# Kernel tuning notes

Hardware: AMD Instinct MI355X
Metric: run time of the kernel (lower is better)

## Reference

```python
import jax, jax.numpy as jnp
import numpy as np

N_HEADS = 4
NEG_SLOPE = 0.2  # DGL GATConv default leaky_relu slope


def setup_inputs() -> dict:
    key = jax.random.key(0)
    ks = jax.random.split(key, 12)
    N, E = 50000, 800000
    in_dim, time_dim, out_dim = 128, 128, 128
    d_head = out_dim // N_HEADS
    in_total = in_dim + time_dim
    h = jax.random.normal(ks[0], (N, in_dim), jnp.float32)
    time_tensor = jax.random.uniform(ks[1], (E,), jnp.float32)
    src = jax.random.randint(ks[2], (E,), 0, N, jnp.int32)
    dst = jax.random.randint(ks[3], (E,), 0, N, jnp.int32)
    # TimeEncoding: Linear(1, time_dim) with xavier weight, zero bias
    w_t = jax.random.normal(ks[4], (time_dim, 1), jnp.float32) * (6.0 / (1 + time_dim)) ** 0.5
    b_t = jnp.zeros((time_dim,), jnp.float32)
    # GATConv params
    W_fc = jax.random.normal(ks[5], (N_HEADS * d_head, in_total), jnp.float32) * (2.0 / in_total) ** 0.5
    attn_l = jax.random.normal(ks[6], (N_HEADS, d_head), jnp.float32) * 0.1
    attn_r = jax.random.normal(ks[7], (N_HEADS, d_head), jnp.float32) * 0.1
    W_res = jax.random.normal(ks[8], (N_HEADS * d_head, in_total), jnp.float32) * (2.0 / in_total) ** 0.5
    bias = jnp.zeros((N_HEADS * d_head,), jnp.float32)
    return {"h": h, "time_tensor": time_tensor, "src": src, "dst": dst,
            "num_nodes": N, "w_t": w_t, "b_t": b_t, "W_fc": W_fc,
            "attn_l": attn_l, "attn_r": attn_r, "W_res": W_res, "bias": bias}


def reference(h, time_tensor, src, dst, num_nodes, w_t, b_t, W_fc, attn_l, attn_r, W_res, bias):
    N = num_nodes
    E = src.shape[0]
    # Time encoding: cos(W t + b), per edge -> [E, time_dim]
    time_emb = jnp.cos(time_tensor[:, None] * w_t[:, 0][None, :] + b_t[None, :])
    # Mailbox mean of concat([src h, time_emb]) per dst node.
    # mean(concat) == concat(mean, mean), so sum the two halves separately.
    ones = jnp.ones((E,), h.dtype)
    deg = jax.ops.segment_sum(ones, dst, num_segments=N)  # [N]
    sum_h = jax.ops.segment_sum(h[src], dst, num_segments=N)       # [N, in_dim]
    sum_t = jax.ops.segment_sum(time_emb, dst, num_segments=N)     # [N, time_dim]
    inv_deg = 1.0 / jnp.maximum(deg, 1.0)
    h_time = jnp.concatenate([sum_h, sum_t], axis=1) * inv_deg[:, None]  # [N, in+time]
    # GATConv (eval mode, no dropout)
    d_head = W_fc.shape[0] // N_HEADS
    feat = (h_time @ W_fc.T).reshape(N, N_HEADS, d_head)  # [N,H,D]
    el = jnp.sum(feat * attn_l[None], axis=-1)  # [N,H]
    er = jnp.sum(feat * attn_r[None], axis=-1)  # [N,H]
    e = el[src] + er[dst]                        # [E,H]
    e = jnp.where(e > 0, e, NEG_SLOPE * e)
    # edge softmax over incoming edges of each dst node
    m = jax.ops.segment_max(e, dst, num_segments=N)  # [N,H]
    m = jnp.where(jnp.isfinite(m), m, 0.0)
    ex = jnp.exp(e - m[dst])
    denom = jax.ops.segment_sum(ex, dst, num_segments=N)
    a = ex / jnp.maximum(denom[dst], 1e-9)           # [E,H]
    rst = jax.ops.segment_sum(a[:, :, None] * feat[src], dst, num_segments=N)  # [N,H,D]
    res = (h_time @ W_res.T).reshape(N, N_HEADS, d_head)
    out = rst + res + bias.reshape(1, N_HEADS, d_head)
    out = jax.nn.elu(out)
    return out.reshape(N, -1)  # [N, out_dim]
```

## Files before the change

### kernel.cpp

```cpp
#include <hip/hip_runtime.h>
#include <math.h>

#define NH 4
#define NEG_SLOPE 0.2f
#define BKT_SHIFT 8
#define EPB 4096
#define CBLK 8192
#define INV2PI 0.15915494309189535f
#define LOG2E  1.4426950408889634f

typedef __attribute__((ext_vector_type(8))) short bf16x8;
typedef __attribute__((ext_vector_type(4))) float f32x4;

__device__ __forceinline__ float blo(unsigned u) { return __uint_as_float(u << 16); }
__device__ __forceinline__ float bhi(unsigned u) { return __uint_as_float(u & 0xFFFF0000u); }
__device__ __forceinline__ unsigned short rne(float f) {
    unsigned u = __float_as_uint(f);
    u += 0x7FFFu + ((u >> 16) & 1u);
    return (unsigned short)(u >> 16);
}
__device__ __forceinline__ unsigned pack2(float a, float b) {
    return (unsigned)rne(a) | ((unsigned)rne(b) << 16);
}

__global__ __launch_bounds__(256) void k_prep(
    const float* __restrict__ h, unsigned* __restrict__ hbu, int n_pairs,
    const float* __restrict__ Wfc, const float* __restrict__ Wres,
    unsigned* __restrict__ wcat,
    const float* __restrict__ w_t, const float* __restrict__ b_t,
    float2* __restrict__ w_s, float2* __restrict__ b_s) {
    int t = blockIdx.x * blockDim.x + threadIdx.x;
    if (t < n_pairs) {
        float2 v = ((const float2*)h)[t];
        hbu[t] = pack2(v.x, v.y);
    }
    if (t < 32768) {
        int col = t >> 7, kk = t & 127;
        const float* srcp = (col < 128) ? (Wfc + (size_t)col * 256)
                                        : (Wres + (size_t)(col - 128) * 256);
        float2 v = ((const float2*)srcp)[kk];
        wcat[t] = pack2(v.x, v.y);
    }
    if (t < 64) {
        float2 wv = ((const float2*)w_t)[t];
        float2 bv = ((const float2*)b_t)[t];
        w_s[t] = make_float2(wv.x * INV2PI, wv.y * INV2PI);
        b_s[t] = make_float2(bv.x * INV2PI, bv.y * INV2PI);
    }
}

__global__ __launch_bounds__(256) void k_bktcount(
    const int* __restrict__ dst, int* __restrict__ bkt_cnt, int E, int NB) {
    __shared__ int cnt[256];
    int tid = threadIdx.x;
    cnt[tid] = 0;
    __syncthreads();
    int q0 = (blockIdx.x * CBLK) >> 2;
#pragma unroll
    for (int k = 0; k < CBLK / 1024; k++) {
        int qi = q0 + k * 256 + tid;
        int base = qi * 4;
        if (base + 3 < E) {
            int4 d = ((const int4*)dst)[qi];
            atomicAdd(&cnt[d.x >> BKT_SHIFT], 1);
            atomicAdd(&cnt[d.y >> BKT_SHIFT], 1);
            atomicAdd(&cnt[d.z >> BKT_SHIFT], 1);
            atomicAdd(&cnt[d.w >> BKT_SHIFT], 1);
        } else {
            for (int e = base; e < E; e++) atomicAdd(&cnt[dst[e] >> BKT_SHIFT], 1);
        }
    }
    __syncthreads();
    if (tid < NB) {
        int c = cnt[tid];
        if (c) atomicAdd(bkt_cnt + tid, c);
    }
}

__global__ __launch_bounds__(256) void k_bktscan(
    const int* __restrict__ bkt_cnt, int* __restrict__ bkt_start,
    int* __restrict__ bkt_cursor, int* __restrict__ row_start,
    int NB, int E, int N) {
    __shared__ int wsum[4];
    int tid = threadIdx.x, lane = tid & 63, wid = tid >> 6;
    int v = (tid < NB) ? bkt_cnt[tid] : 0;
    int x = v;
#pragma unroll
    for (int off = 1; off < 64; off <<= 1) {
        int y = __shfl_up(x, off, 64);
        if (lane >= off) x += y;
    }
    if (lane == 63) wsum[wid] = x;
    __syncthreads();
    if (tid == 0) {
        int s = 0;
#pragma unroll
        for (int k = 0; k < 4; k++) { int tk = wsum[k]; wsum[k] = s; s += tk; }
    }
    __syncthreads();
    int excl = wsum[wid] + x - v;
    if (tid < NB) { bkt_start[tid] = excl; bkt_cursor[tid] = excl; }
    if (tid == 0) { bkt_start[NB] = E; row_start[N] = E; }
}

__global__ __launch_bounds__(256) void k_binscatter(
    const int* __restrict__ src, const int* __restrict__ dst,
    const float* __restrict__ tt, int* __restrict__ bkt_cursor,
    uint2* __restrict__ staged, int E, int NB) {
    __shared__ int cnt[1024];
    __shared__ int basep[1024];
    int e0 = blockIdx.x * EPB;
    int tid = threadIdx.x;
    for (int b = tid; b < NB; b += 256) cnt[b] = 0;
    __syncthreads();
#pragma unroll
    for (int k = 0; k < EPB / 256; k++) {
        int e = e0 + k * 256 + tid;
        if (e < E) atomicAdd(&cnt[dst[e] >> BKT_SHIFT], 1);
    }
    __syncthreads();
    for (int b = tid; b < NB; b += 256) {
        int c = cnt[b];
        basep[b] = (c > 0) ? atomicAdd(bkt_cursor + b, c) : 0;
        cnt[b] = 0;
    }
    __syncthreads();
#pragma unroll
    for (int k = 0; k < EPB / 256; k++) {
        int e = e0 + k * 256 + tid;
        if (e < E) {
            int d = dst[e];
            int b = d >> BKT_SHIFT;
            int r = atomicAdd(&cnt[b], 1);
            unsigned tq = min((unsigned)(tt[e] * 32768.0f), 32767u);
            staged[basep[b] + r] =
                make_uint2(((unsigned)src[e] << 15) | tq, (unsigned)(d & 255));
        }
    }
}

__global__ __launch_bounds__(256) void k_binsort(
    const uint2* __restrict__ staged, const int* __restrict__ bkt_start,
    int* __restrict__ row_start, unsigned* __restrict__ est, int N) {
    __shared__ int cnt[256];
    __shared__ int cur[256];
    __shared__ int wsum[4];
    int b = blockIdx.x;
    int n0 = b << BKT_SHIFT;
    int tid = threadIdx.x;
    cnt[tid] = 0;
    __syncthreads();
    int s0 = bkt_start[b], s1 = bkt_start[b + 1];
    for (int p = s0 + tid; p < s1; p += 256)
        atomicAdd(&cnt[staged[p].y], 1);
    __syncthreads();
    int lane = tid & 63, wid = tid >> 6;
    int v = cnt[tid];
    int x = v;
#pragma unroll
    for (int off = 1; off < 64; off <<= 1) {
        int y = __shfl_up(x, off, 64);
        if (lane >= off) x += y;
    }
    if (lane == 63) wsum[wid] = x;
    __syncthreads();
    if (tid == 0) {
        int s = 0;
#pragma unroll
        for (int k = 0; k < 4; k++) { int tk = wsum[k]; wsum[k] = s; s += tk; }
    }
    __syncthreads();
    int excl = s0 + wsum[wid] + x - v;
    cur[tid] = excl;
    if (n0 + tid < N) row_start[n0 + tid] = excl;
    __syncthreads();
    for (int p = s0 + tid; p < s1; p += 256) {
        uint2 vv = staged[p];
        int pos = atomicAdd(&cur[vv.y], 1);
        est[pos] = vv.x;
    }
}

__device__ __forceinline__ void agg_edge(unsigned u, float wgt, const uint4* __restrict__ h4,
                                         int i, float4 wa, float4 wb, float4 ba, float4 bb,
                                         float* aH, float* aT) {
    int s = (int)(u >> 15);
    float t = (float)((u & 0x7FFFu)) * (1.0f / 32768.0f) + (0.5f / 32768.0f);
    uint4 hv = h4[(size_t)s * 16 + i];
    aH[0] += wgt * blo(hv.x); aH[1] += wgt * bhi(hv.x);
    aH[2] += wgt * blo(hv.y); aH[3] += wgt * bhi(hv.y);
    aH[4] += wgt * blo(hv.z); aH[5] += wgt * bhi(hv.z);
    aH[6] += wgt * blo(hv.w); aH[7] += wgt * bhi(hv.w);
    aT[0] += wgt * __builtin_amdgcn_cosf(fmaf(t, wa.x, ba.x));
    aT[1] += wgt * __builtin_amdgcn_cosf(fmaf(t, wa.y, ba.y));
    aT[2] += wgt * __builtin_amdgcn_cosf(fmaf(t, wa.z, ba.z));
    aT[3] += wgt * __builtin_amdgcn_cosf(fmaf(t, wa.w, ba.w));
    aT[4] += wgt * __builtin_amdgcn_cosf(fmaf(t, wb.x, bb.x));
    aT[5] += wgt * __builtin_amdgcn_cosf(fmaf(t, wb.y, bb.y));
    aT[6] += wgt * __builtin_amdgcn_cosf(fmaf(t, wb.z, bb.z));
    aT[7] += wgt * __builtin_amdgcn_cosf(fmaf(t, wb.w, bb.w));
}

__device__ __forceinline__ void attn_edge(unsigned u, bool valid, const uint4* __restrict__ f4,
                                          int i, int hd, const float* __restrict__ el,
                                          float erh, float* acc, float& den) {
    int s = (int)(u >> 15);
    float elh = el[(size_t)s * 4 + hd];
    uint4 fv = f4[(size_t)s * 16 + i];
    float w = elh + erh; w = w > 0.f ? w : NEG_SLOPE * w;
    float ex = valid ? __builtin_amdgcn_exp2f(w) : 0.f;
    acc[0] = fmaf(ex, blo(fv.x), acc[0]); acc[1] = fmaf(ex, bhi(fv.x), acc[1]);
    acc[2] = fmaf(ex, blo(fv.y), acc[2]); acc[3] = fmaf(ex, bhi(fv.y), acc[3]);
    acc[4] = fmaf(ex, blo(fv.z), acc[4]); acc[5] = fmaf(ex, bhi(fv.z), acc[5]);
    acc[6] = fmaf(ex, blo(fv.w), acc[6]); acc[7] = fmaf(ex, bhi(fv.w), acc[7]);
    den += ex;
}

__global__ __launch_bounds__(256) void k_agg(
    const unsigned* __restrict__ hbu, const unsigned* __restrict__ est,
    const int* __restrict__ row_start,
    const float2* __restrict__ w_s, const float2* __restrict__ b_s,
    unsigned* __restrict__ htu, int N) {
    int n = blockIdx.x * 4 + (threadIdx.x >> 6);
    if (n >= N) return;
    int lane = threadIdx.x & 63;
    int g = lane >> 4, i = lane & 15;
    int rs = row_start[n], re = row_start[n + 1];
    const uint4* h4 = (const uint4*)hbu;
    float4 wa = ((const float4*)w_s)[2 * i], wb = ((const float4*)w_s)[2 * i + 1];
    float4 ba = ((const float4*)b_s)[2 * i], bb = ((const float4*)b_s)[2 * i + 1];
    float aH[8] = {}, aT[8] = {};
    for (int e = rs + g; e < re; e += 16) {
        int e1 = e + 4, e2 = e + 8, e3 = e + 12;
        bool v1 = e1 < re, v2 = e2 < re, v3 = e3 < re;
        unsigned u0 = est[e];
        unsigned u1 = est[v1 ? e1 : e];
        unsigned u2 = est[v2 ? e2 : e];
        unsigned u3 = est[v3 ? e3 : e];
        agg_edge(u0, 1.0f, h4, i, wa, wb, ba, bb, aH, aT);
        agg_edge(u1, v1 ? 1.0f : 0.0f, h4, i, wa, wb, ba, bb, aH, aT);
        agg_edge(u2, v2 ? 1.0f : 0.0f, h4, i, wa, wb, ba, bb, aH, aT);
        agg_edge(u3, v3 ? 1.0f : 0.0f, h4, i, wa, wb, ba, bb, aH, aT);
    }
#pragma unroll
    for (int off = 16; off <= 32; off <<= 1) {
#pragma unroll
        for (int k = 0; k < 8; k++) {
            aH[k] += __shfl_xor(aH[k], off, 64);
            aT[k] += __shfl_xor(aT[k], off, 64);
        }
    }
    if (g == 0) {
        int deg = re - rs;
        float idg = (deg > 0) ? 1.0f / (float)deg : 1.0f;
        uint4* ht4 = (uint4*)htu;
        uint4 oh, ot;
        oh.x = pack2(aH[0] * idg, aH[1] * idg);
        oh.y = pack2(aH[2] * idg, aH[3] * idg);
        oh.z = pack2(aH[4] * idg, aH[5] * idg);
        oh.w = pack2(aH[6] * idg, aH[7] * idg);
        ot.x = pack2(aT[0] * idg, aT[1] * idg);
        ot.y = pack2(aT[2] * idg, aT[3] * idg);
        ot.z = pack2(aT[4] * idg, aT[5] * idg);
        ot.w = pack2(aT[6] * idg, aT[7] * idg);
        ht4[(size_t)n * 32 + i]      = oh;
        ht4[(size_t)n * 32 + 16 + i] = ot;
    }
}

__global__ __launch_bounds__(256) void k_gemm(
    const unsigned short* __restrict__ ht, const unsigned short* __restrict__ wcat,
    unsigned short* __restrict__ feat, float* __restrict__ res_out, int N) {
    __shared__ __align__(16) unsigned short As[64 * 264];
    int tid = threadIdx.x;
    int row0 = blockIdx.x * 64;
    const uint4* src4 = (const uint4*)ht;
    for (int idx = tid; idx < 64 * 32; idx += 256) {
        int rl = idx >> 5, c16 = idx & 31;
        int gr = row0 + rl; if (gr >= N) gr = N - 1;
        uint4 v = src4[(size_t)gr * 32 + c16];
        *(uint4*)(As + rl * 264 + c16 * 8) = v;
    }
    __syncthreads();
    int wave = tid >> 6, lane = tid & 63;
    int r = lane & 15, q = lane >> 4;
    int colbase = wave * 64;
    const bf16x8* bbase = (const bf16x8*)wcat + (size_t)(colbase + r) * 32;
    const unsigned short* abase = As + r * 264 + q * 8;
    f32x4 acc[4][4] = {};
#pragma unroll
    for (int ks = 0; ks < 8; ks++) {
        bf16x8 a[4], b[4];
#pragma unroll
        for (int rt = 0; rt < 4; rt++)
            a[rt] = *(const bf16x8*)(abase + rt * (16 * 264) + ks * 32);
#pragma unroll
        for (int ct = 0; ct < 4; ct++)
            b[ct] = bbase[(size_t)ct * (16 * 32) + ks * 4 + q];
#pragma unroll
        for (int rt = 0; rt < 4; rt++)
#pragma unroll
            for (int ct = 0; ct < 4; ct++)
                acc[rt][ct] = __builtin_amdgcn_mfma_f32_16x16x32_bf16(a[rt], b[ct], acc[rt][ct], 0, 0, 0);
    }
#pragma unroll
    for (int rt = 0; rt < 4; rt++) {
        int rb = row0 + rt * 16 + q * 4;
#pragma unroll
        for (int ct = 0; ct < 4; ct++) {
            int col = colbase + ct * 16 + r;
#pragma unroll
            for (int reg = 0; reg < 4; reg++) {
                int row = rb + reg;
                if (row >= N) continue;
                float v = acc[rt][ct][reg];
                if (col < 128) feat[(size_t)row * 128 + col] = rne(v);
                else           res_out[(size_t)row * 128 + (col - 128)] = v;
            }
        }
    }
}

__global__ void k_el_er(const unsigned* __restrict__ featu,
                        const float* __restrict__ attn_l, const float* __restrict__ attn_r,
                        float* __restrict__ el, float* __restrict__ er, int NH4) {
    int t = blockIdx.x * blockDim.x + threadIdx.x;
    if (t >= NH4) return;
    int n = t >> 2, hd = t & 3;
    const unsigned* f = featu + (size_t)n * 64 + hd * 16;
    const float2* al = (const float2*)(attn_l + hd * 32);
    const float2* ar = (const float2*)(attn_r + hd * 32);
    float sl = 0.f, sr = 0.f;
#pragma unroll
    for (int i = 0; i < 16; i++) {
        unsigned u = f[i];
        float f0 = blo(u), f1 = bhi(u);
        float2 a = al[i], b = ar[i];
        sl = fmaf(f0, a.x, fmaf(f1, a.y, sl));
        sr = fmaf(f0, b.x, fmaf(f1, b.y, sr));
    }
    el[t] = sl * LOG2E;
    er[t] = sr * LOG2E;
}

__global__ __launch_bounds__(256) void k_attn(
    const unsigned* __restrict__ est, const int* __restrict__ row_start,
    const float* __restrict__ el, const float* __restrict__ er,
    const unsigned* __restrict__ featu, const float* __restrict__ bias,
    float* __restrict__ out, int N) {
    int n = blockIdx.x * 4 + (threadIdx.x >> 6);
    if (n >= N) return;
    int lane = threadIdx.x & 63;
    int g = lane >> 4, i = lane & 15;
    int hd = i >> 2;
    int rs = row_start[n], re = row_start[n + 1];
    float erh = er[(size_t)n * 4 + hd];
    const uint4* f4 = (const uint4*)featu;
    float acc[8] = {};
    float den = 0.f;
    for (int e = rs + g; e < re; e += 16) {
        int e1 = e + 4, e2 = e + 8, e3 = e + 12;
        bool v1 = e1 < re, v2 = e2 < re, v3 = e3 < re;
        unsigned u0 = est[e];
        unsigned u1 = est[v1 ? e1 : e];
        unsigned u2 = est[v2 ? e2 : e];
        unsigned u3 = est[v3 ? e3 : e];
        attn_edge(u0, true, f4, i, hd, el, erh, acc, den);
        attn_edge(u1, v1, f4, i, hd, el, erh, acc, den);
        attn_edge(u2, v2, f4, i, hd, el, erh, acc, den);
        attn_edge(u3, v3, f4, i, hd, el, erh, acc, den);
    }
#pragma unroll
    for (int off = 16; off <= 32; off <<= 1) {
#pragma unroll
        for (int k = 0; k < 8; k++) acc[k] += __shfl_xor(acc[k], off, 64);
        den += __shfl_xor(den, off, 64);
    }
    if (g == 0) {
        float id = 1.0f / fmaxf(den, 1e-9f);
        float* op = out + (size_t)n * 128 + i * 8;
        const float* bp = bias + i * 8;
        float4 o0 = ((const float4*)op)[0], o1 = ((const float4*)op)[1];
        float4 b0 = ((const float4*)bp)[0], b1 = ((const float4*)bp)[1];
        float4 r0, r1;
        r0.x = fmaf(acc[0], id, o0.x + b0.x);
        r0.y = fmaf(acc[1], id, o0.y + b0.y);
        r0.z = fmaf(acc[2], id, o0.z + b0.z);
        r0.w = fmaf(acc[3], id, o0.w + b0.w);
        r1.x = fmaf(acc[4], id, o1.x + b1.x);
        r1.y = fmaf(acc[5], id, o1.y + b1.y);
        r1.z = fmaf(acc[6], id, o1.z + b1.z);
        r1.w = fmaf(acc[7], id, o1.w + b1.w);
        r0.x = r0.x > 0.f ? r0.x : (__expf(r0.x) - 1.0f);
        r0.y = r0.y > 0.f ? r0.y : (__expf(r0.y) - 1.0f);
        r0.z = r0.z > 0.f ? r0.z : (__expf(r0.z) - 1.0f);
        r0.w = r0.w > 0.f ? r0.w : (__expf(r0.w) - 1.0f);
        r1.x = r1.x > 0.f ? r1.x : (__expf(r1.x) - 1.0f);
        r1.y = r1.y > 0.f ? r1.y : (__expf(r1.y) - 1.0f);
        r1.z = r1.z > 0.f ? r1.z : (__expf(r1.z) - 1.0f);
        r1.w = r1.w > 0.f ? r1.w : (__expf(r1.w) - 1.0f);
        ((float4*)op)[0] = r0;
        ((float4*)op)[1] = r1;
    }
}

extern "C" void kernel_launch(void* const* d_in, const int* in_sizes, int n_in,
                              void* d_out, int out_size, void* d_ws, size_t ws_size,
                              hipStream_t stream) {
    const float* h     = (const float*)d_in[0];
    const float* tt    = (const float*)d_in[1];
    const int*   src   = (const int*)d_in[2];
    const int*   dst   = (const int*)d_in[3];
    const float* w_t   = (const float*)d_in[5];
    const float* b_t   = (const float*)d_in[6];
    const float* W_fc  = (const float*)d_in[7];
    const float* al    = (const float*)d_in[8];
    const float* ar    = (const float*)d_in[9];
    const float* W_res = (const float*)d_in[10];
    const float* bias  = (const float*)d_in[11];

    int N = in_sizes[0] / 128;
    int E = in_sizes[1];
    int NB = (N + 255) >> BKT_SHIFT;

    char* ws = (char*)d_ws;
    size_t off = 0;
    auto alloc = [&](size_t bytes) { void* p = ws + off; off = (off + bytes + 15) & ~(size_t)15; return p; };
    unsigned* htu     = (unsigned*)alloc((size_t)N * 128 * 4);
    unsigned* hbu     = (unsigned*)alloc((size_t)N * 64 * 4);
    unsigned* featu   = (unsigned*)alloc((size_t)N * 64 * 4);
    unsigned* wcat    = (unsigned*)alloc(32768 * 4);
    float2*   w_s     = (float2*)alloc(64 * 8);
    float2*   b_s     = (float2*)alloc(64 * 8);
    float*    el      = (float*)alloc((size_t)N * NH * 4);
    float*    er      = (float*)alloc((size_t)N * NH * 4);
    int*      row_st  = (int*)alloc((size_t)(N + 1) * 4);
    int*      bkt_cur = (int*)alloc((size_t)NB * 4);
    int*      bkt_cnt = (int*)alloc((size_t)NB * 4);
    int*      bkt_sta = (int*)alloc((size_t)(NB + 1) * 4);
    unsigned* est     = (unsigned*)alloc((size_t)E * 4);
    uint2*    staged  = (uint2*)featu;

    hipMemsetAsync(bkt_cnt, 0, (size_t)NB * 4, stream);

    int prep_n = N * 64;
    hipLaunchKernelGGL(k_prep, dim3((prep_n + 255) / 256), dim3(256), 0, stream,
                       h, hbu, prep_n, W_fc, W_res, wcat, w_t, b_t, w_s, b_s);
    hipLaunchKernelGGL(k_bktcount, dim3((E + CBLK - 1) / CBLK), dim3(256), 0, stream,
                       dst, bkt_cnt, E, NB);
    hipLaunchKernelGGL(k_bktscan, dim3(1), dim3(256), 0, stream,
                       bkt_cnt, bkt_sta, bkt_cur, row_st, NB, E, N);
    hipLaunchKernelGGL(k_binscatter, dim3((E + EPB - 1) / EPB), dim3(256), 0, stream,
                       src, dst, tt, bkt_cur, staged, E, NB);
    hipLaunchKernelGGL(k_binsort, dim3(NB), dim3(256), 0, stream,
                       staged, bkt_sta, row_st, est, N);
    hipLaunchKernelGGL(k_agg, dim3((N + 3) / 4), dim3(256), 0, stream,
                       hbu, est, row_st, w_s, b_s, htu, N);
    hipLaunchKernelGGL(k_gemm, dim3((N + 63) / 64), dim3(256), 0, stream,
                       (const unsigned short*)htu, (const unsigned short*)wcat,
                       (unsigned short*)featu, (float*)d_out, N);
    hipLaunchKernelGGL(k_el_er, dim3((N * NH + 255) / 256), dim3(256), 0, stream,
                       featu, al, ar, el, er, N * NH);
    hipLaunchKernelGGL(k_attn, dim3((N + 3) / 4), dim3(256), 0, stream,
                       est, row_st, el, er, featu, bias, (float*)d_out, N);
}
```

Baseline: 252.2 us.

## Fuse bucket count into prep, el/er into GEMM epilogue, peel edge-loop tails

Folds the dst-bucket histogram into the prep kernel and computes the el/er attention logits inside the GEMM epilogue using shuffle reductions. This removes two kernel launches and one pass over feat. The agg and attn edge loops now run full 16-edge groups without per-edge validity masks, then handle the leftover edges in a separate tail loop. The cost is extra shuffle work in the GEMM epilogue and more divergent control flow in prep.

```diff
diff --git a/kernel.cpp b/kernel.cpp
--- a/kernel.cpp
+++ b/kernel.cpp
@@ -28,8 +28,11 @@
     const float* __restrict__ Wfc, const float* __restrict__ Wres,
     unsigned* __restrict__ wcat,
     const float* __restrict__ w_t, const float* __restrict__ b_t,
-    float2* __restrict__ w_s, float2* __restrict__ b_s) {
-    int t = blockIdx.x * blockDim.x + threadIdx.x;
+    float2* __restrict__ w_s, float2* __restrict__ b_s,
+    const int* __restrict__ dst, int* __restrict__ bkt_cnt, int E, int NB, int EB) {
+    __shared__ int cnt[256];
+    int tid = threadIdx.x;
+    int t = blockIdx.x * blockDim.x + tid;
     if (t < n_pairs) {
         float2 v = ((const float2*)h)[t];
         hbu[t] = pack2(v.x, v.y);
@@ -47,33 +50,29 @@
         w_s[t] = make_float2(wv.x * INV2PI, wv.y * INV2PI);
         b_s[t] = make_float2(bv.x * INV2PI, bv.y * INV2PI);
     }
-}
-
-__global__ __launch_bounds__(256) void k_bktcount(
-    const int* __restrict__ dst, int* __restrict__ bkt_cnt, int E, int NB) {
-    __shared__ int cnt[256];
-    int tid = threadIdx.x;
-    cnt[tid] = 0;
-    __syncthreads();
-    int q0 = (blockIdx.x * CBLK) >> 2;
-#pragma unroll
-    for (int k = 0; k < CBLK / 1024; k++) {
-        int qi = q0 + k * 256 + tid;
-        int base = qi * 4;
-        if (base + 3 < E) {
-            int4 d = ((const int4*)dst)[qi];
-            atomicAdd(&cnt[d.x >> BKT_SHIFT], 1);
-            atomicAdd(&cnt[d.y >> BKT_SHIFT], 1);
-            atomicAdd(&cnt[d.z >> BKT_SHIFT], 1);
-            atomicAdd(&cnt[d.w >> BKT_SHIFT], 1);
-        } else {
-            for (int e = base; e < E; e++) atomicAdd(&cnt[dst[e] >> BKT_SHIFT], 1);
-        }
-    }
-    __syncthreads();
-    if (tid < NB) {
-        int c = cnt[tid];
-        if (c) atomicAdd(bkt_cnt + tid, c);
+    if (blockIdx.x < (unsigned)EB) {
+        cnt[tid] = 0;
+        __syncthreads();
+        int q0 = (blockIdx.x * CBLK) >> 2;
+#pragma unroll
+        for (int k = 0; k < CBLK / 1024; k++) {
+            int qi = q0 + k * 256 + tid;
+            int base = qi * 4;
+            if (base + 3 < E) {
+                int4 d = ((const int4*)dst)[qi];
+                atomicAdd(&cnt[d.x >> BKT_SHIFT], 1);
+                atomicAdd(&cnt[d.y >> BKT_SHIFT], 1);
+                atomicAdd(&cnt[d.z >> BKT_SHIFT], 1);
+                atomicAdd(&cnt[d.w >> BKT_SHIFT], 1);
+            } else {
+                for (int e = base; e < E; e++) atomicAdd(&cnt[dst[e] >> BKT_SHIFT], 1);
+            }
+        }
+        __syncthreads();
+        if (tid < NB) {
+            int c = cnt[tid];
+            if (c) atomicAdd(bkt_cnt + tid, c);
+        }
     }
 }
 
@@ -181,34 +180,34 @@
     }
 }
 
-__device__ __forceinline__ void agg_edge(unsigned u, float wgt, const uint4* __restrict__ h4,
+__device__ __forceinline__ void agg_edge(unsigned u, const uint4* __restrict__ h4,
                                          int i, float4 wa, float4 wb, float4 ba, float4 bb,
                                          float* aH, float* aT) {
     int s = (int)(u >> 15);
     float t = (float)((u & 0x7FFFu)) * (1.0f / 32768.0f) + (0.5f / 32768.0f);
     uint4 hv = h4[(size_t)s * 16 + i];
-    aH[0] += wgt * blo(hv.x); aH[1] += wgt * bhi(hv.x);
-    aH[2] += wgt * blo(hv.y); aH[3] += wgt * bhi(hv.y);
-    aH[4] += wgt * blo(hv.z); aH[5] += wgt * bhi(hv.z);
-    aH[6] += wgt * blo(hv.w); aH[7] += wgt * bhi(hv.w);
-    aT[0] += wgt * __builtin_amdgcn_cosf(fmaf(t, wa.x, ba.x));
-    aT[1] += wgt * __builtin_amdgcn_cosf(fmaf(t, wa.y, ba.y));
-    aT[2] += wgt * __builtin_amdgcn_cosf(fmaf(t, wa.z, ba.z));
-    aT[3] += wgt * __builtin_amdgcn_cosf(fmaf(t, wa.w, ba.w));
-    aT[4] += wgt * __builtin_amdgcn_cosf(fmaf(t, wb.x, bb.x));
-    aT[5] += wgt * __builtin_amdgcn_cosf(fmaf(t, wb.y, bb.y));
-    aT[6] += wgt * __builtin_amdgcn_cosf(fmaf(t, wb.z, bb.z));
-    aT[7] += wgt * __builtin_amdgcn_cosf(fmaf(t, wb.w, bb.w));
-}
-
-__device__ __forceinline__ void attn_edge(unsigned u, bool valid, const uint4* __restrict__ f4,
+    aH[0] += blo(hv.x); aH[1] += bhi(hv.x);
+    aH[2] += blo(hv.y); aH[3] += bhi(hv.y);
+    aH[4] += blo(hv.z); aH[5] += bhi(hv.z);
+    aH[6] += blo(hv.w); aH[7] += bhi(hv.w);
+    aT[0] += __builtin_amdgcn_cosf(fmaf(t, wa.x, ba.x));
+    aT[1] += __builtin_amdgcn_cosf(fmaf(t, wa.y, ba.y));
+    aT[2] += __builtin_amdgcn_cosf(fmaf(t, wa.z, ba.z));
+    aT[3] += __builtin_amdgcn_cosf(fmaf(t, wa.w, ba.w));
+    aT[4] += __builtin_amdgcn_cosf(fmaf(t, wb.x, bb.x));
+    aT[5] += __builtin_amdgcn_cosf(fmaf(t, wb.y, bb.y));
+    aT[6] += __builtin_amdgcn_cosf(fmaf(t, wb.z, bb.z));
+    aT[7] += __builtin_amdgcn_cosf(fmaf(t, wb.w, bb.w));
+}
+
+__device__ __forceinline__ void attn_edge(unsigned u, const uint4* __restrict__ f4,
                                           int i, int hd, const float* __restrict__ el,
                                           float erh, float* acc, float& den) {
     int s = (int)(u >> 15);
     float elh = el[(size_t)s * 4 + hd];
     uint4 fv = f4[(size_t)s * 16 + i];
     float w = elh + erh; w = w > 0.f ? w : NEG_SLOPE * w;
-    float ex = valid ? __builtin_amdgcn_exp2f(w) : 0.f;
+    float ex = __builtin_amdgcn_exp2f(w);
     acc[0] = fmaf(ex, blo(fv.x), acc[0]); acc[1] = fmaf(ex, bhi(fv.x), acc[1]);
     acc[2] = fmaf(ex, blo(fv.y), acc[2]); acc[3] = fmaf(ex, bhi(fv.y), acc[3]);
     acc[4] = fmaf(ex, blo(fv.z), acc[4]); acc[5] = fmaf(ex, bhi(fv.z), acc[5]);
@@ -230,18 +229,20 @@
     float4 wa = ((const float4*)w_s)[2 * i], wb = ((const float4*)w_s)[2 * i + 1];
     float4 ba = ((const float4*)b_s)[2 * i], bb = ((const float4*)b_s)[2 * i + 1];
     float aH[8] = {}, aT[8] = {};
-    for (int e = rs + g; e < re; e += 16) {
-        int e1 = e + 4, e2 = e + 8, e3 = e + 12;
-        bool v1 = e1 < re, v2 = e2 < re, v3 = e3 < re;
+    int nb = (re - rs) >> 4;
+    int e = rs + g;
+    for (int j = 0; j < nb; j++, e += 16) {
         unsigned u0 = est[e];
-        unsigned u1 = est[v1 ? e1 : e];
-        unsigned u2 = est[v2 ? e2 : e];
-        unsigned u3 = est[v3 ? e3 : e];
-        agg_edge(u0, 1.0f, h4, i, wa, wb, ba, bb, aH, aT);
-        agg_edge(u1, v1 ? 1.0f : 0.0f, h4, i, wa, wb, ba, bb, aH, aT);
-        agg_edge(u2, v2 ? 1.0f : 0.0f, h4, i, wa, wb, ba, bb, aH, aT);
-        agg_edge(u3, v3 ? 1.0f : 0.0f, h4, i, wa, wb, ba, bb, aH, aT);
-    }
+        unsigned u1 = est[e + 4];
+        unsigned u2 = est[e + 8];
+        unsigned u3 = est[e + 12];
+        agg_edge(u0, h4, i, wa, wb, ba, bb, aH, aT);
+        agg_edge(u1, h4, i, wa, wb, ba, bb, aH, aT);
+        agg_edge(u2, h4, i, wa, wb, ba, bb, aH, aT);
+        agg_edge(u3, h4, i, wa, wb, ba, bb, aH, aT);
+    }
+    for (; e < re; e += 4)
+        agg_edge(est[e], h4, i, wa, wb, ba, bb, aH, aT);
 #pragma unroll
     for (int off = 16; off <= 32; off <<= 1) {
 #pragma unroll
@@ -270,7 +271,9 @@
 
 __global__ __launch_bounds__(256) void k_gemm(
     const unsigned short* __restrict__ ht, const unsigned short* __restrict__ wcat,
-    unsigned short* __restrict__ feat, float* __restrict__ res_out, int N) {
+    unsigned short* __restrict__ feat, float* __restrict__ res_out,
+    const float* __restrict__ attn_l, const float* __restrict__ attn_r,
+    float* __restrict__ el, float* __restrict__ er, int N) {
     __shared__ __align__(16) unsigned short As[64 * 264];
     int tid = threadIdx.x;
     int row0 = blockIdx.x * 64;
@@ -303,44 +306,53 @@
             for (int ct = 0; ct < 4; ct++)
                 acc[rt][ct] = __builtin_amdgcn_mfma_f32_16x16x32_bf16(a[rt], b[ct], acc[rt][ct], 0, 0, 0);
     }
+    bool featw = (colbase < 128);
+    float alv[4], arv[4];
+    if (featw) {
+#pragma unroll
+        for (int ct = 0; ct < 4; ct++) {
+            alv[ct] = attn_l[colbase + ct * 16 + r];
+            arv[ct] = attn_r[colbase + ct * 16 + r];
+        }
+    }
 #pragma unroll
     for (int rt = 0; rt < 4; rt++) {
-        int rb = row0 + rt * 16 + q * 4;
-#pragma unroll
-        for (int ct = 0; ct < 4; ct++) {
-            int col = colbase + ct * 16 + r;
-#pragma unroll
-            for (int reg = 0; reg < 4; reg++) {
-                int row = rb + reg;
-                if (row >= N) continue;
+#pragma unroll
+        for (int reg = 0; reg < 4; reg++) {
+            int row = row0 + rt * 16 + q * 4 + reg;
+            float el0 = 0.f, el1 = 0.f, er0 = 0.f, er1 = 0.f;
+#pragma unroll
+            for (int ct = 0; ct < 4; ct++) {
+                int col = colbase + ct * 16 + r;
                 float v = acc[rt][ct][reg];
-                if (col < 128) feat[(size_t)row * 128 + col] = rne(v);
-                else           res_out[(size_t)row * 128 + (col - 128)] = v;
+                if (featw) {
+                    unsigned short pv = rne(v);
+                    if (row < N) feat[(size_t)row * 128 + col] = pv;
+                    float vr = blo((unsigned)pv);
+                    if (ct < 2) { el0 = fmaf(vr, alv[ct], el0); er0 = fmaf(vr, arv[ct], er0); }
+                    else        { el1 = fmaf(vr, alv[ct], el1); er1 = fmaf(vr, arv[ct], er1); }
+                } else {
+                    if (row < N) res_out[(size_t)row * 128 + (col - 128)] = v;
+                }
             }
-        }
-    }
-}
-
-__global__ void k_el_er(const unsigned* __restrict__ featu,
-                        const float* __restrict__ attn_l, const float* __restrict__ attn_r,
-                        float* __restrict__ el, float* __restrict__ er, int NH4) {
-    int t = blockIdx.x * blockDim.x + threadIdx.x;
-    if (t >= NH4) return;
-    int n = t >> 2, hd = t & 3;
-    const unsigned* f = featu + (size_t)n * 64 + hd * 16;
-    const float2* al = (const float2*)(attn_l + hd * 32);
-    const float2* ar = (const float2*)(attn_r + hd * 32);
-    float sl = 0.f, sr = 0.f;
-#pragma unroll
-    for (int i = 0; i < 16; i++) {
-        unsigned u = f[i];
-        float f0 = blo(u), f1 = bhi(u);
-        float2 a = al[i], b = ar[i];
-        sl = fmaf(f0, a.x, fmaf(f1, a.y, sl));
-        sr = fmaf(f0, b.x, fmaf(f1, b.y, sr));
-    }
-    el[t] = sl * LOG2E;
-    er[t] = sr * LOG2E;
+            if (featw) {
+#pragma unroll
+                for (int off = 1; off <= 8; off <<= 1) {
+                    el0 += __shfl_xor(el0, off, 64);
+                    el1 += __shfl_xor(el1, off, 64);
+                    er0 += __shfl_xor(er0, off, 64);
+                    er1 += __shfl_xor(er1, off, 64);
+                }
+                if (r == 0 && row < N) {
+                    int hd0 = colbase >> 5;
+                    el[(size_t)row * 4 + hd0]     = el0 * LOG2E;
+                    el[(size_t)row * 4 + hd0 + 1] = el1 * LOG2E;
+                    er[(size_t)row * 4 + hd0]     = er0 * LOG2E;
+                    er[(size_t)row * 4 + hd0 + 1] = er1 * LOG2E;
+                }
+            }
+        }
+    }
 }
 
 __global__ __launch_bounds__(256) void k_attn(
@@ -358,18 +370,20 @@
     const uint4* f4 = (const uint4*)featu;
     float acc[8] = {};
     float den = 0.f;
-    for (int e = rs + g; e < re; e += 16) {
-        int e1 = e + 4, e2 = e + 8, e3 = e + 12;
-        bool v1 = e1 < re, v2 = e2 < re, v3 = e3 < re;
+    int nb = (re - rs) >> 4;
+    int e = rs + g;
+    for (int j = 0; j < nb; j++, e += 16) {
         unsigned u0 = est[e];
-        unsigned u1 = est[v1 ? e1 : e];
-        unsigned u2 = est[v2 ? e2 : e];
-        unsigned u3 = est[v3 ? e3 : e];
-        attn_edge(u0, true, f4, i, hd, el, erh, acc, den);
-        attn_edge(u1, v1, f4, i, hd, el, erh, acc, den);
-        attn_edge(u2, v2, f4, i, hd, el, erh, acc, den);
-        attn_edge(u3, v3, f4, i, hd, el, erh, acc, den);
-    }
+        unsigned u1 = est[e + 4];
+        unsigned u2 = est[e + 8];
+        unsigned u3 = est[e + 12];
+        attn_edge(u0, f4, i, hd, el, erh, acc, den);
+        attn_edge(u1, f4, i, hd, el, erh, acc, den);
+        attn_edge(u2, f4, i, hd, el, erh, acc, den);
+        attn_edge(u3, f4, i, hd, el, erh, acc, den);
+    }
+    for (; e < re; e += 4)
+        attn_edge(est[e], f4, i, hd, el, erh, acc, den);
 #pragma unroll
     for (int off = 16; off <= 32; off <<= 1) {
 #pragma unroll
@@ -422,6 +436,7 @@
     int N = in_sizes[0] / 128;
     int E = in_sizes[1];
     int NB = (N + 255) >> BKT_SHIFT;
+    int EB = (E + CBLK - 1) / CBLK;
 
     char* ws = (char*)d_ws;
     size_t off = 0;
@@ -445,9 +460,8 @@
 
     int prep_n = N * 64;
     hipLaunchKernelGGL(k_prep, dim3((prep_n + 255) / 256), dim3(256), 0, stream,
-                       h, hbu, prep_n, W_fc, W_res, wcat, w_t, b_t, w_s, b_s);
-    hipLaunchKernelGGL(k_bktcount, dim3((E + CBLK - 1) / CBLK), dim3(256), 0, stream,
-                       dst, bkt_cnt, E, NB);
+                       h, hbu, prep_n, W_fc, W_res, wcat, w_t, b_t, w_s, b_s,
+                       dst, bkt_cnt, E, NB, EB);
     hipLaunchKernelGGL(k_bktscan, dim3(1), dim3(256), 0, stream,
                        bkt_cnt, bkt_sta, bkt_cur, row_st, NB, E, N);
     hipLaunchKernelGGL(k_binscatter, dim3((E + EPB - 1) / EPB), dim3(256), 0, stream,
@@ -458,9 +472,7 @@
                        hbu, est, row_st, w_s, b_s, htu, N);
     hipLaunchKernelGGL(k_gemm, dim3((N + 63) / 64), dim3(256), 0, stream,
                        (const unsigned short*)htu, (const unsigned short*)wcat,
-                       (unsigned short*)featu, (float*)d_out, N);
-    hipLaunchKernelGGL(k_el_er, dim3((N * NH + 255) / 256), dim3(256), 0, stream,
-                       featu, al, ar, el, er, N * NH);
+                       (unsigned short*)featu, (float*)d_out, al, ar, el, er, N);
     hipLaunchKernelGGL(k_attn, dim3((N + 3) / 4), dim3(256), 0, stream,
                        est, row_st, el, er, featu, bias, (float*)d_out, N);
 }
```

Measured after the change: 252.1 us. About the same (-0.0%).
